# Performance work log

Hardware: AMD Instinct MI355X
Metric: run time of the kernel (lower is better)

The kernel has to match this reference:

```python
import jax, jax.numpy as jnp
import numpy as np

B, L, C, H, Wd = 256, 64, 256, 32, 32  # batch, num_filts, code_dim, height, width

def setup_inputs() -> dict:
    key = jax.random.key(0)
    k1, k2 = jax.random.split(key)
    code = jax.random.normal(k1, (B, L, C), dtype=jnp.float32)
    # stacked per-filter weights: weights[l].weight has shape [code_dim, H*W]
    W = jax.random.normal(k2, (L, C, H * Wd), dtype=jnp.float32) * (1.0 / np.sqrt(C))
    return {"code": code, "W": W}

def reference(code, W):
    # Original: for each filter l, x_hat[:, l] = code[:, l, :] @ weights[l].weight
    # (F.linear(x, weight.t()) == x @ weight). Fuse into one batched GEMM.
    # code: [B, L, C], W: [L, C, HW] -> out: [B, L, HW]
    x_hat = jnp.einsum('blc,lcd->bld', code, W)
    return x_hat.reshape(code.shape[0], W.shape[0], H, Wd)
```

## Files before the change

kernel.cpp:

```cpp
#include <hip/hip_runtime.h>
#include <hip/hip_bf16.h>

#define B_  256
#define L_  64
#define C_  256
#define HW_ 1024

typedef float  floatx4 __attribute__((ext_vector_type(4)));
typedef __bf16 bf16x8  __attribute__((ext_vector_type(8)));
typedef __bf16 bf16x4  __attribute__((ext_vector_type(4)));
typedef __bf16 bf16x2  __attribute__((ext_vector_type(2)));

#define LDA_ROW 80
#define LDB_ROW 64

#define BARRIER_LDS() asm volatile("s_waitcnt lgkmcnt(0)\n\ts_barrier" ::: "memory")

__device__ __forceinline__ int g2(int n) { return (n ^ (n >> 2)) & 3; }

__global__ __launch_bounds__(1024, 4)
void gld_mfma_kernel(const float* __restrict__ code,
                     const float* __restrict__ W,
                     float* __restrict__ out)
{
    const int tid = threadIdx.x;

    const int id   = blockIdx.x;
    const int ll   = id & 7;
    const int rest = id >> 3;
    const int n0   = (rest & 3) * 256;
    const int l    = (rest >> 2) * 8 + ll;

    __shared__ unsigned char Alds[2][256 * LDA_ROW];
    __shared__ unsigned char Blds[2][256 * LDB_ROW];

    const int lane = tid & 63;
    const int wave = tid >> 6;
    const int wm = (wave >> 2) * 64;
    const int wn = (wave & 3) * 64;

    floatx4 acc[4][4];
    #pragma unroll
    for (int i = 0; i < 4; ++i)
        #pragma unroll
        for (int j = 0; j < 4; ++j)
            acc[i][j] = (floatx4)0.0f;

    const int a_row = tid >> 2;
    const int a_k4  = (tid & 3) * 4;
    const int b_i = tid & 63;

    const float* aBase = code + (size_t)l * C_ + a_k4;
    const float* wBase = W + (size_t)l * (C_ * HW_) + (size_t)(2 * wave) * HW_ + n0 + 4 * b_i;

    floatx4 Areg[2][2];
    floatx4 Breg[2][2];

    Areg[0][0] = *(const floatx4*)(aBase + (size_t)a_row * (L_ * C_));
    Areg[0][1] = *(const floatx4*)(aBase + (size_t)a_row * (L_ * C_) + 16);
    #pragma unroll
    for (int r = 0; r < 2; ++r)
        Breg[0][r] = *(const floatx4*)(wBase + (size_t)r * HW_);

    int bwaddr[4];
    #pragma unroll
    for (int j = 0; j < 4; ++j) {
        const int row = 4 * b_i + j;
        bwaddr[j] = row * LDB_ROW + ((((wave >> 2) ^ g2(row))) << 4) + ((wave & 3) << 2);
    }
    const int awaddr = a_row * LDA_ROW + 2 * a_k4;

    #pragma unroll
    for (int t = 0; t < 8; ++t) {
        const int s  = t & 1;
        const int kb = t * 32;

        if (t < 7) {
            Areg[s ^ 1][0] = *(const floatx4*)(aBase + (size_t)a_row * (L_ * C_) + (kb + 32));
            Areg[s ^ 1][1] = *(const floatx4*)(aBase + (size_t)a_row * (L_ * C_) + (kb + 48));
            #pragma unroll
            for (int r = 0; r < 2; ++r)
                Breg[s ^ 1][r] = *(const floatx4*)(wBase + (size_t)(kb + 32 + r) * HW_);
        }

        if (t > 0) {
            const unsigned char* Ab = Alds[s ^ 1];
            const unsigned char* Bb = Blds[s ^ 1];
            bf16x8 af[4], bfr[4];
            const int c16 = lane >> 4;
            #pragma unroll
            for (int i = 0; i < 4; ++i)
                af[i] = *(const bf16x8*)&Ab[(wm + i * 16 + (lane & 15)) * LDA_ROW + c16 * 16];
            #pragma unroll
            for (int j = 0; j < 4; ++j) {
                const int n = wn + j * 16 + (lane & 15);
                bfr[j] = *(const bf16x8*)&Bb[n * LDB_ROW + ((c16 ^ g2(n)) << 4)];
            }
            #pragma unroll
            for (int i = 0; i < 4; ++i)
                #pragma unroll
                for (int j = 0; j < 4; ++j)
                    acc[i][j] = __builtin_amdgcn_mfma_f32_16x16x32_bf16(af[i], bfr[j], acc[i][j], 0, 0, 0);
        }

        #pragma unroll
        for (int j = 0; j < 4; ++j) {
            bf16x2 h;
            h.x = (__bf16)Breg[s][0][j];
            h.y = (__bf16)Breg[s][1][j];
            *(bf16x2*)&Blds[s][bwaddr[j]] = h;
        }
        #pragma unroll
        for (int p = 0; p < 2; ++p) {
            bf16x4 h;
            h.x = (__bf16)Areg[s][p].x; h.y = (__bf16)Areg[s][p].y;
            h.z = (__bf16)Areg[s][p].z; h.w = (__bf16)Areg[s][p].w;
            *(bf16x4*)&Alds[s][awaddr + p * 32] = h;
        }

        BARRIER_LDS();
    }

    {
        const unsigned char* Ab = Alds[1];
        const unsigned char* Bb = Blds[1];
        bf16x8 af[4], bfr[4];
        const int c16 = lane >> 4;
        #pragma unroll
        for (int i = 0; i < 4; ++i)
            af[i] = *(const bf16x8*)&Ab[(wm + i * 16 + (lane & 15)) * LDA_ROW + c16 * 16];
        #pragma unroll
        for (int j = 0; j < 4; ++j) {
            const int n = wn + j * 16 + (lane & 15);
            bfr[j] = *(const bf16x8*)&Bb[n * LDB_ROW + ((c16 ^ g2(n)) << 4)];
        }
        #pragma unroll
        for (int i = 0; i < 4; ++i)
            #pragma unroll
            for (int j = 0; j < 4; ++j)
                acc[i][j] = __builtin_amdgcn_mfma_f32_16x16x32_bf16(af[i], bfr[j], acc[i][j], 0, 0, 0);
    }

    const int col0 = lane & 15;
    const int row0 = (lane >> 4) * 4;
    #pragma unroll
    for (int i = 0; i < 4; ++i) {
        #pragma unroll
        for (int j = 0; j < 4; ++j) {
            const int m = wm + i * 16 + row0;
            const int n = n0 + wn + j * 16 + col0;
            float* o = out + (size_t)m * (L_ * HW_) + (size_t)l * HW_ + n;
            #pragma unroll
            for (int r = 0; r < 4; ++r)
                o[(size_t)r * (L_ * HW_)] = acc[i][j][r];
        }
    }
}

extern "C" void kernel_launch(void* const* d_in, const int* in_sizes, int n_in,
                              void* d_out, int out_size, void* d_ws, size_t ws_size,
                              hipStream_t stream) {
    const float* code = (const float*)d_in[0];
    const float* W    = (const float*)d_in[1];
    float* out        = (float*)d_out;

    gld_mfma_kernel<<<dim3(256), 1024, 0, stream>>>(code, W, out);
}
```

Before: 124.7 us.

## Prefetch W two stages ahead and remap B-load thread layout with new swizzle

Result: slower. 134.9 us (+8.2%).

```diff
diff --git a/kernel.cpp b/kernel.cpp
--- a/kernel.cpp
+++ b/kernel.cpp
@@ -16,7 +16,7 @@
 
 #define BARRIER_LDS() asm volatile("s_waitcnt lgkmcnt(0)\n\ts_barrier" ::: "memory")
 
-__device__ __forceinline__ int g2(int n) { return (n ^ (n >> 2)) & 3; }
+__device__ __forceinline__ int g2x(int n) { return ((n >> 1) ^ (n >> 3)) & 3; }
 
 __global__ __launch_bounds__(1024, 4)
 void gld_mfma_kernel(const float* __restrict__ code,
@@ -48,44 +48,50 @@
 
     const int a_row = tid >> 2;
     const int a_k4  = (tid & 3) * 4;
-    const int b_i = tid & 63;
+    const int b_kp = tid & 15;
+    const int b_i  = tid >> 4;
 
     const float* aBase = code + (size_t)l * C_ + a_k4;
-    const float* wBase = W + (size_t)l * (C_ * HW_) + (size_t)(2 * wave) * HW_ + n0 + 4 * b_i;
+    const float* wBase = W + (size_t)l * (C_ * HW_) + (size_t)(2 * b_kp) * HW_ + n0 + 4 * b_i;
 
     floatx4 Areg[2][2];
-    floatx4 Breg[2][2];
+    floatx4 Breg[3][2];
 
     Areg[0][0] = *(const floatx4*)(aBase + (size_t)a_row * (L_ * C_));
     Areg[0][1] = *(const floatx4*)(aBase + (size_t)a_row * (L_ * C_) + 16);
     #pragma unroll
     for (int r = 0; r < 2; ++r)
         Breg[0][r] = *(const floatx4*)(wBase + (size_t)r * HW_);
+    #pragma unroll
+    for (int r = 0; r < 2; ++r)
+        Breg[1][r] = *(const floatx4*)(wBase + (size_t)(32 + r) * HW_);
 
     int bwaddr[4];
     #pragma unroll
     for (int j = 0; j < 4; ++j) {
         const int row = 4 * b_i + j;
-        bwaddr[j] = row * LDB_ROW + ((((wave >> 2) ^ g2(row))) << 4) + ((wave & 3) << 2);
+        bwaddr[j] = row * LDB_ROW + ((((b_kp >> 2) ^ g2x(row))) << 4) + ((b_kp & 3) << 2);
     }
     const int awaddr = a_row * LDA_ROW + 2 * a_k4;
 
     #pragma unroll
     for (int t = 0; t < 8; ++t) {
-        const int s  = t & 1;
+        const int sb = t & 1;
         const int kb = t * 32;
 
         if (t < 7) {
-            Areg[s ^ 1][0] = *(const floatx4*)(aBase + (size_t)a_row * (L_ * C_) + (kb + 32));
-            Areg[s ^ 1][1] = *(const floatx4*)(aBase + (size_t)a_row * (L_ * C_) + (kb + 48));
+            Areg[sb ^ 1][0] = *(const floatx4*)(aBase + (size_t)a_row * (L_ * C_) + (kb + 32));
+            Areg[sb ^ 1][1] = *(const floatx4*)(aBase + (size_t)a_row * (L_ * C_) + (kb + 48));
+        }
+        if (t < 6) {
             #pragma unroll
             for (int r = 0; r < 2; ++r)
-                Breg[s ^ 1][r] = *(const floatx4*)(wBase + (size_t)(kb + 32 + r) * HW_);
+                Breg[(t + 2) % 3][r] = *(const floatx4*)(wBase + (size_t)(kb + 64 + r) * HW_);
         }
 
         if (t > 0) {
-            const unsigned char* Ab = Alds[s ^ 1];
-            const unsigned char* Bb = Blds[s ^ 1];
+            const unsigned char* Ab = Alds[sb ^ 1];
+            const unsigned char* Bb = Blds[sb ^ 1];
             bf16x8 af[4], bfr[4];
             const int c16 = lane >> 4;
             #pragma unroll
@@ -94,7 +100,7 @@
             #pragma unroll
             for (int j = 0; j < 4; ++j) {
                 const int n = wn + j * 16 + (lane & 15);
-                bfr[j] = *(const bf16x8*)&Bb[n * LDB_ROW + ((c16 ^ g2(n)) << 4)];
+                bfr[j] = *(const bf16x8*)&Bb[n * LDB_ROW + ((c16 ^ g2x(n)) << 4)];
             }
             #pragma unroll
             for (int i = 0; i < 4; ++i)
@@ -103,19 +109,22 @@
                     acc[i][j] = __builtin_amdgcn_mfma_f32_16x16x32_bf16(af[i], bfr[j], acc[i][j], 0, 0, 0);
         }
 
-        #pragma unroll
-        for (int j = 0; j < 4; ++j) {
-            bf16x2 h;
-            h.x = (__bf16)Breg[s][0][j];
-            h.y = (__bf16)Breg[s][1][j];
-            *(bf16x2*)&Blds[s][bwaddr[j]] = h;
+        {
+            const int r3 = t % 3;
+            #pragma unroll
+            for (int j = 0; j < 4; ++j) {
+                bf16x2 h;
+                h.x = (__bf16)Breg[r3][0][j];
+                h.y = (__bf16)Breg[r3][1][j];
+                *(bf16x2*)&Blds[sb][bwaddr[j]] = h;
+            }
         }
         #pragma unroll
         for (int p = 0; p < 2; ++p) {
             bf16x4 h;
-            h.x = (__bf16)Areg[s][p].x; h.y = (__bf16)Areg[s][p].y;
-            h.z = (__bf16)Areg[s][p].z; h.w = (__bf16)Areg[s][p].w;
-            *(bf16x4*)&Alds[s][awaddr + p * 32] = h;
+            h.x = (__bf16)Areg[sb][p].x; h.y = (__bf16)Areg[sb][p].y;
+            h.z = (__bf16)Areg[sb][p].z; h.w = (__bf16)Areg[sb][p].w;
+            *(bf16x4*)&Alds[sb][awaddr + p * 32] = h;
         }
 
         BARRIER_LDS();
@@ -132,7 +141,7 @@
         #pragma unroll
         for (int j = 0; j < 4; ++j) {
             const int n = wn + j * 16 + (lane & 15);
-            bfr[j] = *(const bf16x8*)&Bb[n * LDB_ROW + ((c16 ^ g2(n)) << 4)];
+            bfr[j] = *(const bf16x8*)&Bb[n * LDB_ROW + ((c16 ^ g2x(n)) << 4)];
         }
         #pragma unroll
         for (int i = 0; i < 4; ++i)
```
